# Performance work log

Hardware: AMD Instinct MI355X
Metric: run time of the kernel (lower is better)

The kernel has to match this reference:

```python
import jax, jax.numpy as jnp
import numpy as np

EMBED_DIM = 1024
NUM_HEADS = 16
HEAD_DIM = EMBED_DIM // NUM_HEADS
SCALE = HEAD_DIM ** -0.5
B, S = 2, 2048


def setup_inputs() -> dict:
    key = jax.random.key(0)
    ks = jax.random.split(key, 10)
    def lin(kw, kb, fan_in):
        bound = 1.0 / np.sqrt(fan_in)
        W = jax.random.uniform(kw, (EMBED_DIM, EMBED_DIM), jnp.float32, -bound, bound)
        b = jax.random.uniform(kb, (EMBED_DIM,), jnp.float32, -bound, bound)
        return W, b
    Wq, bq = lin(ks[0], ks[1], EMBED_DIM)
    Wk, bk = lin(ks[2], ks[3], EMBED_DIM)
    Wv, bv = lin(ks[4], ks[5], EMBED_DIM)
    Wo, bo = lin(ks[6], ks[7], EMBED_DIM)
    x = jax.random.normal(ks[8], (B, S, EMBED_DIM), jnp.float32)
    # sparsity_mask: True where token kept (rand > sparsity with sparsity=0.5)
    sparsity_mask = jax.random.randint(ks[9], (B, NUM_HEADS, S), 0, 2).astype(bool)
    return {"x": x, "sparsity_mask": sparsity_mask,
            "Wq": Wq, "bq": bq, "Wk": Wk, "bk": bk,
            "Wv": Wv, "bv": bv, "Wo": Wo, "bo": bo}


def reference(x, sparsity_mask, Wq, bq, Wk, bk, Wv, bv, Wo, bo):
    b, s, _ = x.shape
    def heads(W, bias):
        # torch Linear: x @ W.T + b ; then [b, s, h, d] -> [b, h, s, d]
        y = x @ W.T + bias
        return y.reshape(b, s, NUM_HEADS, HEAD_DIM).transpose(0, 2, 1, 3)
    q = heads(Wq, bq)
    k = heads(Wk, bk)
    v = heads(Wv, bv)
    m = sparsity_mask[..., None].astype(q.dtype)  # [b, h, s, 1]
    q = q * m
    k = k * m
    attn = jnp.einsum('bhqd,bhkd->bhqk', q, k) * SCALE
    attn = jax.nn.softmax(attn, axis=-1)
    out = jnp.einsum('bhqk,bhkd->bhqd', attn, v)
    out = out.transpose(0, 2, 1, 3).reshape(b, s, EMBED_DIM)
    return out @ Wo.T + bo
```

## Files before the change

kernel.cpp:

```cpp
#include <hip/hip_runtime.h>

#define DEV __device__ __forceinline__

typedef __bf16 bf16x8 __attribute__((ext_vector_type(8)));
typedef __bf16 bf16x4 __attribute__((ext_vector_type(4)));
typedef float f32x4 __attribute__((ext_vector_type(4)));
typedef unsigned u32x4 __attribute__((ext_vector_type(4)));
typedef unsigned short ushort_t;

static constexpr int EMBED = 1024;
static constexpr int NHEAD = 16;
static constexpr int HDIM  = 64;
static constexpr int S_    = 2048;
static constexpr float SCALE_L2E = 0.125f * 1.44269504088896340736f;

DEV ushort_t f2bf(float f) {
  unsigned u = __builtin_bit_cast(unsigned, f);
  unsigned r = (u + 0x7fffu + ((u >> 16) & 1u)) >> 16;
  return (ushort_t)r;
}

#define GLOAD_LDS16(g, l)                                                   \
  __builtin_amdgcn_global_load_lds(                                         \
      (const __attribute__((address_space(1))) unsigned int*)(g),           \
      (__attribute__((address_space(3))) unsigned int*)(l), 16, 0, 0)

#define DRAIN_VM() asm volatile("s_waitcnt vmcnt(0)" ::: "memory")

__global__ __launch_bounds__(256) void convert_kernel(
    const float* __restrict__ x,
    const float* __restrict__ wq, const float* __restrict__ wk,
    const float* __restrict__ wv, const float* __restrict__ wo,
    ushort_t* __restrict__ xb, ushort_t* __restrict__ wqb,
    ushort_t* __restrict__ wkb, ushort_t* __restrict__ wvb,
    ushort_t* __restrict__ wob) {
  size_t i = ((size_t)blockIdx.x * blockDim.x + threadIdx.x) * 4;
  const float* src; ushort_t* dst; size_t off;
  if (i < 4194304u)      { src = x;  dst = xb;  off = i; }
  else if (i < 5242880u) { src = wq; dst = wqb; off = i - 4194304u; }
  else if (i < 6291456u) { src = wk; dst = wkb; off = i - 5242880u; }
  else if (i < 7340032u) { src = wv; dst = wvb; off = i - 6291456u; }
  else                   { src = wo; dst = wob; off = i - 7340032u; }
  float4 v = *(const float4*)(src + off);
  ushort4 o;
  o.x = f2bf(v.x); o.y = f2bf(v.y); o.z = f2bf(v.z); o.w = f2bf(v.w);
  *(ushort4*)(dst + off) = o;
}

__global__ __launch_bounds__(256) void qkv_kernel(
    const ushort_t* __restrict__ xb, const ushort_t* __restrict__ wqb,
    const ushort_t* __restrict__ wkb, const ushort_t* __restrict__ wvb,
    const float* __restrict__ bq, const float* __restrict__ bk,
    const float* __restrict__ bv, const int* __restrict__ mask,
    ushort_t* __restrict__ qo, ushort_t* __restrict__ ko,
    ushort_t* __restrict__ vto) {
  __shared__ __align__(16) unsigned char ldsA[16384];
  __shared__ __align__(16) unsigned char ldsB[16384];
  __shared__ float maskf[2][128];

  const int bid  = blockIdx.x;
  const int tid  = threadIdx.x;
  const int lane = tid & 63;
  const int w    = tid >> 6;
  const int wm   = (w >> 1) * 64;
  const int wn   = (w & 1) * 64;
  const int rl   = lane & 15;
  const int kg   = lane >> 4;

  int mode, ar0, br0;
  const ushort_t *A, *Bm;
  const float* bias;
  if (bid < 512) {
    mode = bid >> 8;
    int t = bid & 255;
    ar0 = (t & 31) * 128;
    br0 = (t >> 5) * 128;
    A = xb; Bm = mode ? wkb : wqb; bias = mode ? bk : bq;
  } else {
    mode = 2;
    int t = bid - 512;
    ar0 = (t & 7) * 128;
    br0 = (t >> 3) * 128;
    A = wvb; Bm = xb; bias = bv;
  }

  if (mode < 2) {
    int hl = tid >> 7, sl = tid & 127;
    int m = ar0 + sl;
    int b = m >> 11, s = m & 2047;
    int h = (br0 >> 6) + hl;
    maskf[hl][sl] = (float)mask[((size_t)b * NHEAD + h) * S_ + s];
  }

  f32x4 acc[4][4];
#pragma unroll
  for (int i = 0; i < 4; ++i)
#pragma unroll
    for (int j = 0; j < 4; ++j) acc[i][j] = f32x4{0.f, 0.f, 0.f, 0.f};

  auto STAGE = [&](int kt) {
    const int k0 = kt * 64;
#pragma unroll
    for (int s = 0; s < 8; ++s) {
      const int basev = s * 256 + w * 64;
      const int Lb = basev & 1023;
      const int L = Lb + lane;
      const int row = L >> 3;
      const int gu = (L & 7) ^ (row & 7);
      if (s < 4) {
        GLOAD_LDS16(A + (size_t)(ar0 + row) * EMBED + k0 + gu * 8, &ldsA[Lb * 16]);
      } else {
        GLOAD_LDS16(Bm + (size_t)(br0 + row) * EMBED + k0 + gu * 8, &ldsB[Lb * 16]);
      }
    }
  };

  for (int kt = 0; kt < 16; ++kt) {
    if (kt) __syncthreads();
    STAGE(kt);
    DRAIN_VM();
    __syncthreads();
#pragma unroll
    for (int kk = 0; kk < 2; ++kk) {
      bf16x8 af[4], bfr[4];
#pragma unroll
      for (int mb = 0; mb < 4; ++mb) {
        const int row = wm + mb * 16 + rl;
        const int off = (kk * 64 + kg * 16) ^ ((row & 7) << 4);
        af[mb] = *(const bf16x8*)(ldsA + row * 128 + off);
      }
#pragma unroll
      for (int nb = 0; nb < 4; ++nb) {
        const int row = wn + nb * 16 + rl;
        const int off = (kk * 64 + kg * 16) ^ ((row & 7) << 4);
        bfr[nb] = *(const bf16x8*)(ldsB + row * 128 + off);
      }
#pragma unroll
      for (int mb = 0; mb < 4; ++mb)
#pragma unroll
        for (int nb = 0; nb < 4; ++nb)
          acc[mb][nb] = __builtin_amdgcn_mfma_f32_16x16x32_bf16(
              af[mb], bfr[nb], acc[mb][nb], 0, 0, 0);
    }
  }

#pragma unroll
  for (int mb = 0; mb < 4; ++mb)
#pragma unroll
    for (int nb = 0; nb < 4; ++nb)
#pragma unroll
      for (int r = 0; r < 4; ++r) {
        int row_l = wm + mb * 16 + kg * 4 + r;
        int col_l = wn + nb * 16 + rl;
        float v = acc[mb][nb][r];
        if (mode < 2) {
          int m = ar0 + row_l, n = br0 + col_l;
          v = (v + bias[n]) * maskf[col_l >> 6][row_l];
          if (mode == 0) v *= SCALE_L2E;
          int b = m >> 11, s = m & 2047, h = n >> 6, d = n & 63;
          ushort_t* o = mode ? ko : qo;
          o[(((size_t)(b * NHEAD + h)) * S_ + s) * HDIM + d] = f2bf(v);
        } else {
          int n = ar0 + row_l, m = br0 + col_l;
          v += bias[n];
          int b = m >> 11, s = m & 2047, h = n >> 6, d = n & 63;
          vto[(((size_t)(b * NHEAD + h)) * HDIM + d) * S_ + s] = f2bf(v);
        }
      }
}

__global__ __launch_bounds__(256) void gemm_o_kernel(
    const ushort_t* __restrict__ A, const ushort_t* __restrict__ Bm,
    const float* __restrict__ bias, float* __restrict__ outp) {
  __shared__ __align__(16) unsigned char ldsA[16384];
  __shared__ __align__(16) unsigned char ldsB[16384];

  const int tid  = threadIdx.x;
  const int lane = tid & 63;
  const int w    = tid >> 6;
  const int ar0  = blockIdx.x * 128;
  const int br0  = blockIdx.y * 128;
  const int wm   = (w >> 1) * 64;
  const int wn   = (w & 1) * 64;
  const int rl   = lane & 15;
  const int kg   = lane >> 4;

  f32x4 acc[4][4];
#pragma unroll
  for (int i = 0; i < 4; ++i)
#pragma unroll
    for (int j = 0; j < 4; ++j) acc[i][j] = f32x4{0.f, 0.f, 0.f, 0.f};

  auto STAGE = [&](int kt) {
    const int k0 = kt * 64;
#pragma unroll
    for (int s = 0; s < 8; ++s) {
      const int basev = s * 256 + w * 64;
      const int Lb = basev & 1023;
      const int L = Lb + lane;
      const int row = L >> 3;
      const int gu = (L & 7) ^ (row & 7);
      if (s < 4) {
        GLOAD_LDS16(A + (size_t)(ar0 + row) * EMBED + k0 + gu * 8, &ldsA[Lb * 16]);
      } else {
        GLOAD_LDS16(Bm + (size_t)(br0 + row) * EMBED + k0 + gu * 8, &ldsB[Lb * 16]);
      }
    }
  };

  for (int kt = 0; kt < 16; ++kt) {
    if (kt) __syncthreads();
    STAGE(kt);
    DRAIN_VM();
    __syncthreads();
#pragma unroll
    for (int kk = 0; kk < 2; ++kk) {
      bf16x8 af[4], bfr[4];
#pragma unroll
      for (int mb = 0; mb < 4; ++mb) {
        const int row = wm + mb * 16 + rl;
        const int off = (kk * 64 + kg * 16) ^ ((row & 7) << 4);
        af[mb] = *(const bf16x8*)(ldsA + row * 128 + off);
      }
#pragma unroll
      for (int nb = 0; nb < 4; ++nb) {
        const int row = wn + nb * 16 + rl;
        const int off = (kk * 64 + kg * 16) ^ ((row & 7) << 4);
        bfr[nb] = *(const bf16x8*)(ldsB + row * 128 + off);
      }
#pragma unroll
      for (int mb = 0; mb < 4; ++mb)
#pragma unroll
        for (int nb = 0; nb < 4; ++nb)
          acc[mb][nb] = __builtin_amdgcn_mfma_f32_16x16x32_bf16(
              af[mb], bfr[nb], acc[mb][nb], 0, 0, 0);
    }
  }

#pragma unroll
  for (int mb = 0; mb < 4; ++mb)
#pragma unroll
    for (int nb = 0; nb < 4; ++nb)
#pragma unroll
      for (int r = 0; r < 4; ++r) {
        int m = ar0 + wm + mb * 16 + kg * 4 + r;
        int n = br0 + wn + nb * 16 + rl;
        outp[(size_t)m * EMBED + n] = acc[mb][nb][r] + bias[n];
      }
}

__global__ __launch_bounds__(256) void attn_kernel(
    const ushort_t* __restrict__ qp, const ushort_t* __restrict__ kp,
    const ushort_t* __restrict__ vtp, ushort_t* __restrict__ ao) {
  __shared__ __align__(16) unsigned char ldsK[3][8192];
  __shared__ __align__(16) unsigned char ldsV[3][8192];
  __shared__ __align__(16) unsigned char ldsP[4][4096];

  const int bid  = blockIdx.x;
  const int bh   = (bid & 7) * 4 + (bid >> 7);
  const int qt   = (bid >> 3) & 15;
  const int tid  = threadIdx.x;
  const int lane = tid & 63;
  const int w    = tid >> 6;
  const int q0   = qt * 128 + w * 32;
  const int rl   = lane & 15;
  const int kg   = lane >> 4;
  const int pswz = (rl & 7) << 4;

  const bf16x8 ones = __builtin_bit_cast(bf16x8,
      u32x4{0x3F803F80u, 0x3F803F80u, 0x3F803F80u, 0x3F803F80u});

  bf16x8 qa[2][2];
#pragma unroll
  for (int qb = 0; qb < 2; ++qb)
#pragma unroll
    for (int kk = 0; kk < 2; ++kk)
      qa[qb][kk] = *(const bf16x8*)(qp + ((size_t)bh * S_ + q0 + qb * 16 + rl) * HDIM +
                                    kk * 32 + kg * 8);

  f32x4 o_acc[2][4];
  f32x4 o_l[2];
#pragma unroll
  for (int qb = 0; qb < 2; ++qb) {
#pragma unroll
    for (int nb = 0; nb < 4; ++nb) o_acc[qb][nb] = f32x4{0.f, 0.f, 0.f, 0.f};
    o_l[qb] = f32x4{0.f, 0.f, 0.f, 0.f};
  }

  unsigned char* pb = ldsP[w];

  auto STAGE = [&](int kt, int slot) {
#pragma unroll
    for (int s = 0; s < 4; ++s) {
      const int Lb = (s & 1) * 256 + w * 64;
      const int L = Lb + lane;
      const int row = L >> 3;
      const int gu = (L & 7) ^ (row & 7);
      if (s < 2) {
        GLOAD_LDS16(kp + ((size_t)bh * S_ + (size_t)kt * 64 + row) * HDIM + gu * 8,
                    &ldsK[slot][Lb * 16]);
      } else {
        GLOAD_LDS16(vtp + ((size_t)bh * HDIM + row) * S_ + (size_t)kt * 64 + gu * 8,
                    &ldsV[slot][Lb * 16]);
      }
    }
  };

  STAGE(0, 0);
  STAGE(1, 1);
  asm volatile("s_waitcnt vmcnt(4) lgkmcnt(0)" ::: "memory");
  __builtin_amdgcn_s_barrier();
  int cur = 0;
  for (int kt = 0; kt < 32; ++kt) {
    if (kt + 2 < 32) {
      int slot = cur + 2; if (slot >= 3) slot -= 3;
      STAGE(kt + 2, slot);
    }

    f32x4 sa[2][4];
#pragma unroll
    for (int qb = 0; qb < 2; ++qb)
#pragma unroll
      for (int nb = 0; nb < 4; ++nb) sa[qb][nb] = f32x4{0.f, 0.f, 0.f, 0.f};
    __builtin_amdgcn_s_setprio(1);
#pragma unroll
    for (int nb = 0; nb < 4; ++nb) {
      const int row = nb * 16 + rl;
#pragma unroll
      for (int kk = 0; kk < 2; ++kk) {
        bf16x8 kf = *(const bf16x8*)(ldsK[cur] + row * 128 +
                                     ((kk * 64 + kg * 16) ^ ((row & 7) << 4)));
        sa[0][nb] = __builtin_amdgcn_mfma_f32_16x16x32_bf16(kf, qa[0][kk], sa[0][nb], 0, 0, 0);
        sa[1][nb] = __builtin_amdgcn_mfma_f32_16x16x32_bf16(kf, qa[1][kk], sa[1][nb], 0, 0, 0);
      }
    }
    __builtin_amdgcn_s_setprio(0);

#pragma unroll
    for (int qb = 0; qb < 2; ++qb)
#pragma unroll
      for (int nb = 0; nb < 4; ++nb) {
        bf16x4 pk4;
#pragma unroll
        for (int r = 0; r < 4; ++r)
          pk4[r] = (__bf16)__builtin_amdgcn_exp2f(sa[qb][nb][r]);
        *(bf16x4*)(pb + (qb * 16 + rl) * 128 + ((nb * 32 + kg * 8) ^ pswz)) = pk4;
      }
    asm volatile("s_waitcnt lgkmcnt(0)" ::: "memory");
    __builtin_amdgcn_sched_barrier(0);

    bf16x8 pa[2][2];
#pragma unroll
    for (int qb = 0; qb < 2; ++qb)
#pragma unroll
      for (int kk = 0; kk < 2; ++kk)
        pa[qb][kk] = *(const bf16x8*)(pb + (qb * 16 + rl) * 128 +
                                      ((kk * 64 + kg * 16) ^ pswz));

    __builtin_amdgcn_s_setprio(1);
    o_l[0] = __builtin_amdgcn_mfma_f32_16x16x32_bf16(pa[0][0], ones, o_l[0], 0, 0, 0);
    o_l[0] = __builtin_amdgcn_mfma_f32_16x16x32_bf16(pa[0][1], ones, o_l[0], 0, 0, 0);
    o_l[1] = __builtin_amdgcn_mfma_f32_16x16x32_bf16(pa[1][0], ones, o_l[1], 0, 0, 0);
    o_l[1] = __builtin_amdgcn_mfma_f32_16x16x32_bf16(pa[1][1], ones, o_l[1], 0, 0, 0);

#pragma unroll
    for (int nb = 0; nb < 4; ++nb) {
      const int row = nb * 16 + rl;
#pragma unroll
      for (int kk = 0; kk < 2; ++kk) {
        bf16x8 vb = *(const bf16x8*)(ldsV[cur] + row * 128 +
                                     ((kk * 64 + kg * 16) ^ ((row & 7) << 4)));
        o_acc[0][nb] = __builtin_amdgcn_mfma_f32_16x16x32_bf16(pa[0][kk], vb, o_acc[0][nb], 0, 0, 0);
        o_acc[1][nb] = __builtin_amdgcn_mfma_f32_16x16x32_bf16(pa[1][kk], vb, o_acc[1][nb], 0, 0, 0);
      }
    }
    __builtin_amdgcn_s_setprio(0);

    if (kt + 2 < 32) {
      asm volatile("s_waitcnt vmcnt(4) lgkmcnt(0)" ::: "memory");
    } else {
      asm volatile("s_waitcnt vmcnt(0) lgkmcnt(0)" ::: "memory");
    }
    __builtin_amdgcn_s_barrier();
    cur = (cur == 2) ? 0 : cur + 1;
  }

  const int b = bh >> 4, h = bh & 15;
#pragma unroll
  for (int qb = 0; qb < 2; ++qb)
#pragma unroll
    for (int r = 0; r < 4; ++r) {
      float linv = 1.0f / o_l[qb][r];
      const int row = q0 + qb * 16 + kg * 4 + r;
#pragma unroll
      for (int nb = 0; nb < 4; ++nb) {
        float v = o_acc[qb][nb][r] * linv;
        ao[((size_t)b * S_ + row) * EMBED + h * HDIM + nb * 16 + rl] = f2bf(v);
      }
    }
}

extern "C" void kernel_launch(void* const* d_in, const int* in_sizes, int n_in,
                              void* d_out, int out_size, void* d_ws, size_t ws_size,
                              hipStream_t stream) {
  const float* x    = (const float*)d_in[0];
  const int*   mask = (const int*)d_in[1];
  const float* Wq   = (const float*)d_in[2];
  const float* bq   = (const float*)d_in[3];
  const float* Wk   = (const float*)d_in[4];
  const float* bk   = (const float*)d_in[5];
  const float* Wv   = (const float*)d_in[6];
  const float* bv   = (const float*)d_in[7];
  const float* Wo   = (const float*)d_in[8];
  const float* bo   = (const float*)d_in[9];

  char* ws = (char*)d_ws;
  ushort_t* xb  = (ushort_t*)(ws);
  ushort_t* wqb = (ushort_t*)(ws + 8388608);
  ushort_t* wkb = (ushort_t*)(ws + 10485760);
  ushort_t* wvb = (ushort_t*)(ws + 12582912);
  ushort_t* wob = (ushort_t*)(ws + 14680064);
  ushort_t* qb  = (ushort_t*)(ws + 16777216);
  ushort_t* kb  = (ushort_t*)(ws + 25165824);
  ushort_t* vtb = (ushort_t*)(ws + 33554432);
  ushort_t* aob = (ushort_t*)(ws + 41943040);

  hipLaunchKernelGGL(convert_kernel, dim3(8192), dim3(256), 0, stream,
                     x, Wq, Wk, Wv, Wo, xb, wqb, wkb, wvb, wob);
  hipLaunchKernelGGL(qkv_kernel, dim3(768), dim3(256), 0, stream,
                     xb, wqb, wkb, wvb, bq, bk, bv, mask, qb, kb, vtb);
  hipLaunchKernelGGL(attn_kernel, dim3(512), dim3(256), 0, stream,
                     qb, kb, vtb, aob);
  hipLaunchKernelGGL(gemm_o_kernel, dim3(32, 8), dim3(256), 0, stream,
                     aob, wob, bo, (float*)d_out);
}
```

Measured before the change: 117.2 us.

## Split attention work across 8 waves with 16 query rows each

The attention kernel now launches 512 threads per block, and each of the 8 waves owns 16 query rows instead of 32. K/V staging is spread across the 8 waves, with each issuing one K and one V load per tile, and the vmcnt waits are adjusted to match. This raises the number of waves available to hide latency. In exchange, each K/V fragment read from LDS is reused by fewer MFMAs, so LDS read traffic per FLOP doubles.

```diff
diff --git a/kernel.cpp b/kernel.cpp
--- a/kernel.cpp
+++ b/kernel.cpp
@@ -249,12 +249,12 @@
       }
 }
 
-__global__ __launch_bounds__(256) void attn_kernel(
+__global__ __launch_bounds__(512) void attn_kernel(
     const ushort_t* __restrict__ qp, const ushort_t* __restrict__ kp,
     const ushort_t* __restrict__ vtp, ushort_t* __restrict__ ao) {
   __shared__ __align__(16) unsigned char ldsK[3][8192];
   __shared__ __align__(16) unsigned char ldsV[3][8192];
-  __shared__ __align__(16) unsigned char ldsP[4][4096];
+  __shared__ __align__(16) unsigned char ldsP[8][2048];
 
   const int bid  = blockIdx.x;
   const int bh   = (bid & 7) * 4 + (bid >> 7);
@@ -262,7 +262,7 @@
   const int tid  = threadIdx.x;
   const int lane = tid & 63;
   const int w    = tid >> 6;
-  const int q0   = qt * 128 + w * 32;
+  const int q0   = qt * 128 + w * 16;
   const int rl   = lane & 15;
   const int kg   = lane >> 4;
   const int pswz = (rl & 7) << 4;
@@ -270,45 +270,39 @@
   const bf16x8 ones = __builtin_bit_cast(bf16x8,
       u32x4{0x3F803F80u, 0x3F803F80u, 0x3F803F80u, 0x3F803F80u});
 
-  bf16x8 qa[2][2];
-#pragma unroll
-  for (int qb = 0; qb < 2; ++qb)
-#pragma unroll
-    for (int kk = 0; kk < 2; ++kk)
-      qa[qb][kk] = *(const bf16x8*)(qp + ((size_t)bh * S_ + q0 + qb * 16 + rl) * HDIM +
-                                    kk * 32 + kg * 8);
-
-  f32x4 o_acc[2][4];
-  f32x4 o_l[2];
-#pragma unroll
-  for (int qb = 0; qb < 2; ++qb) {
-#pragma unroll
-    for (int nb = 0; nb < 4; ++nb) o_acc[qb][nb] = f32x4{0.f, 0.f, 0.f, 0.f};
-    o_l[qb] = f32x4{0.f, 0.f, 0.f, 0.f};
-  }
+  bf16x8 qa[2];
+#pragma unroll
+  for (int kk = 0; kk < 2; ++kk)
+    qa[kk] = *(const bf16x8*)(qp + ((size_t)bh * S_ + q0 + rl) * HDIM +
+                              kk * 32 + kg * 8);
+
+  f32x4 o_acc[4];
+  f32x4 o_l = f32x4{0.f, 0.f, 0.f, 0.f};
+#pragma unroll
+  for (int nb = 0; nb < 4; ++nb) o_acc[nb] = f32x4{0.f, 0.f, 0.f, 0.f};
 
   unsigned char* pb = ldsP[w];
 
   auto STAGE = [&](int kt, int slot) {
 #pragma unroll
-    for (int s = 0; s < 4; ++s) {
-      const int Lb = (s & 1) * 256 + w * 64;
+    for (int s = 0; s < 2; ++s) {
+      const int Lb = w * 64;
       const int L = Lb + lane;
       const int row = L >> 3;
       const int gu = (L & 7) ^ (row & 7);
-      if (s < 2) {
+      if (s == 0) {
         GLOAD_LDS16(kp + ((size_t)bh * S_ + (size_t)kt * 64 + row) * HDIM + gu * 8,
-                    &ldsK[slot][Lb * 16]);
+                    &ldsK[slot][L * 16]);
       } else {
         GLOAD_LDS16(vtp + ((size_t)bh * HDIM + row) * S_ + (size_t)kt * 64 + gu * 8,
-                    &ldsV[slot][Lb * 16]);
+                    &ldsV[slot][L * 16]);
       }
     }
   };
 
   STAGE(0, 0);
   STAGE(1, 1);
-  asm volatile("s_waitcnt vmcnt(4) lgkmcnt(0)" ::: "memory");
+  asm volatile("s_waitcnt vmcnt(2) lgkmcnt(0)" ::: "memory");
   __builtin_amdgcn_s_barrier();
   int cur = 0;
   for (int kt = 0; kt < 32; ++kt) {
@@ -317,11 +311,9 @@
       STAGE(kt + 2, slot);
     }
 
-    f32x4 sa[2][4];
-#pragma unroll
-    for (int qb = 0; qb < 2; ++qb)
-#pragma unroll
-      for (int nb = 0; nb < 4; ++nb) sa[qb][nb] = f32x4{0.f, 0.f, 0.f, 0.f};
+    f32x4 sa[4];
+#pragma unroll
+    for (int nb = 0; nb < 4; ++nb) sa[nb] = f32x4{0.f, 0.f, 0.f, 0.f};
     __builtin_amdgcn_s_setprio(1);
 #pragma unroll
     for (int nb = 0; nb < 4; ++nb) {
@@ -330,38 +322,30 @@
       for (int kk = 0; kk < 2; ++kk) {
         bf16x8 kf = *(const bf16x8*)(ldsK[cur] + row * 128 +
                                      ((kk * 64 + kg * 16) ^ ((row & 7) << 4)));
-        sa[0][nb] = __builtin_amdgcn_mfma_f32_16x16x32_bf16(kf, qa[0][kk], sa[0][nb], 0, 0, 0);
-        sa[1][nb] = __builtin_amdgcn_mfma_f32_16x16x32_bf16(kf, qa[1][kk], sa[1][nb], 0, 0, 0);
+        sa[nb] = __builtin_amdgcn_mfma_f32_16x16x32_bf16(kf, qa[kk], sa[nb], 0, 0, 0);
       }
     }
     __builtin_amdgcn_s_setprio(0);
 
 #pragma unroll
-    for (int qb = 0; qb < 2; ++qb)
-#pragma unroll
-      for (int nb = 0; nb < 4; ++nb) {
-        bf16x4 pk4;
-#pragma unroll
-        for (int r = 0; r < 4; ++r)
-          pk4[r] = (__bf16)__builtin_amdgcn_exp2f(sa[qb][nb][r]);
-        *(bf16x4*)(pb + (qb * 16 + rl) * 128 + ((nb * 32 + kg * 8) ^ pswz)) = pk4;
-      }
+    for (int nb = 0; nb < 4; ++nb) {
+      bf16x4 pk4;
+#pragma unroll
+      for (int r = 0; r < 4; ++r)
+        pk4[r] = (__bf16)__builtin_amdgcn_exp2f(sa[nb][r]);
+      *(bf16x4*)(pb + rl * 128 + ((nb * 32 + kg * 8) ^ pswz)) = pk4;
+    }
     asm volatile("s_waitcnt lgkmcnt(0)" ::: "memory");
     __builtin_amdgcn_sched_barrier(0);
 
-    bf16x8 pa[2][2];
-#pragma unroll
-    for (int qb = 0; qb < 2; ++qb)
-#pragma unroll
-      for (int kk = 0; kk < 2; ++kk)
-        pa[qb][kk] = *(const bf16x8*)(pb + (qb * 16 + rl) * 128 +
-                                      ((kk * 64 + kg * 16) ^ pswz));
+    bf16x8 pa[2];
+#pragma unroll
+    for (int kk = 0; kk < 2; ++kk)
+      pa[kk] = *(const bf16x8*)(pb + rl * 128 + ((kk * 64 + kg * 16) ^ pswz));
 
     __builtin_amdgcn_s_setprio(1);
-    o_l[0] = __builtin_amdgcn_mfma_f32_16x16x32_bf16(pa[0][0], ones, o_l[0], 0, 0, 0);
-    o_l[0] = __builtin_amdgcn_mfma_f32_16x16x32_bf16(pa[0][1], ones, o_l[0], 0, 0, 0);
-    o_l[1] = __builtin_amdgcn_mfma_f32_16x16x32_bf16(pa[1][0], ones, o_l[1], 0, 0, 0);
-    o_l[1] = __builtin_amdgcn_mfma_f32_16x16x32_bf16(pa[1][1], ones, o_l[1], 0, 0, 0);
+    o_l = __builtin_amdgcn_mfma_f32_16x16x32_bf16(pa[0], ones, o_l, 0, 0, 0);
+    o_l = __builtin_amdgcn_mfma_f32_16x16x32_bf16(pa[1], ones, o_l, 0, 0, 0);
 
 #pragma unroll
     for (int nb = 0; nb < 4; ++nb) {
@@ -370,14 +354,13 @@
       for (int kk = 0; kk < 2; ++kk) {
         bf16x8 vb = *(const bf16x8*)(ldsV[cur] + row * 128 +
                                      ((kk * 64 + kg * 16) ^ ((row & 7) << 4)));
-        o_acc[0][nb] = __builtin_amdgcn_mfma_f32_16x16x32_bf16(pa[0][kk], vb, o_acc[0][nb], 0, 0, 0);
-        o_acc[1][nb] = __builtin_amdgcn_mfma_f32_16x16x32_bf16(pa[1][kk], vb, o_acc[1][nb], 0, 0, 0);
+        o_acc[nb] = __builtin_amdgcn_mfma_f32_16x16x32_bf16(pa[kk], vb, o_acc[nb], 0, 0, 0);
       }
     }
     __builtin_amdgcn_s_setprio(0);
 
     if (kt + 2 < 32) {
-      asm volatile("s_waitcnt vmcnt(4) lgkmcnt(0)" ::: "memory");
+      asm volatile("s_waitcnt vmcnt(2) lgkmcnt(0)" ::: "memory");
     } else {
       asm volatile("s_waitcnt vmcnt(0) lgkmcnt(0)" ::: "memory");
     }
@@ -387,17 +370,15 @@
 
   const int b = bh >> 4, h = bh & 15;
 #pragma unroll
-  for (int qb = 0; qb < 2; ++qb)
-#pragma unroll
-    for (int r = 0; r < 4; ++r) {
-      float linv = 1.0f / o_l[qb][r];
-      const int row = q0 + qb * 16 + kg * 4 + r;
-#pragma unroll
-      for (int nb = 0; nb < 4; ++nb) {
-        float v = o_acc[qb][nb][r] * linv;
-        ao[((size_t)b * S_ + row) * EMBED + h * HDIM + nb * 16 + rl] = f2bf(v);
-      }
-    }
+  for (int r = 0; r < 4; ++r) {
+    float linv = 1.0f / o_l[r];
+    const int row = q0 + kg * 4 + r;
+#pragma unroll
+    for (int nb = 0; nb < 4; ++nb) {
+      float v = o_acc[nb][r] * linv;
+      ao[((size_t)b * S_ + row) * EMBED + h * HDIM + nb * 16 + rl] = f2bf(v);
+    }
+  }
 }
 
 extern "C" void kernel_launch(void* const* d_in, const int* in_sizes, int n_in,
@@ -429,7 +410,7 @@
                      x, Wq, Wk, Wv, Wo, xb, wqb, wkb, wvb, wob);
   hipLaunchKernelGGL(qkv_kernel, dim3(768), dim3(256), 0, stream,
                      xb, wqb, wkb, wvb, bq, bk, bv, mask, qb, kb, vtb);
-  hipLaunchKernelGGL(attn_kernel, dim3(512), dim3(256), 0, stream,
+  hipLaunchKernelGGL(attn_kernel, dim3(512), dim3(512), 0, stream,
                      qb, kb, vtb, aob);
   hipLaunchKernelGGL(gemm_o_kernel, dim3(32, 8), dim3(256), 0, stream,
                      aob, wob, bo, (float*)d_out);
```

Measured after the change: 115.2 us. No clear change (-1.7%).
